# Optimization experiments

Hardware: AMD Instinct MI355X
Metric: run time of the kernel (lower is better)

The kernel has to match this reference:

```python
import jax, jax.numpy as jnp
import numpy as np

IMG_H = IMG_W = 640.0
NB, NE, NA = 120, 8, 12
L_OBJ, L_BOX, L_HEAD, L_ATTR = 1.0, 5.0, 2.0, 1.0
IGN = -100


def _smooth_l1(p, t):
    d = jnp.abs(p - t)
    return jnp.where(d < 1.0, 0.5 * d * d, d - 0.5)


def _safe_ce(logits, tgt, num_classes):
    # cross-entropy per object, zero where target == ignore_index
    logp = jax.nn.log_softmax(logits, axis=-1)
    ts = jnp.clip(tgt, 0, num_classes - 1).astype(jnp.int32)
    ce = -jnp.take_along_axis(logp, ts[..., None], axis=-1)[..., 0]
    return jnp.where(tgt == IGN, 0.0, ce)


def _scale_box(bx):
    # boxes with max coord <= 1.5 are normalized -> scale to pixels
    sc = jnp.array([IMG_W, IMG_H, IMG_W, IMG_H], dtype=bx.dtype)
    is_norm = jnp.max(bx, axis=-1, keepdims=True) <= 1.5
    return jnp.where(is_norm, bx * sc, bx)


def _per_scale(pred, body_boxes, head_boxes, labels, emotions, actions, head_valid):
    B, H, W, _ = pred.shape
    N = body_boxes.shape[1]
    sx, sy = IMG_W / W, IMG_H / H

    bb = _scale_box(body_boxes)
    x1, y1, x2, y2 = bb[..., 0], bb[..., 1], bb[..., 2], bb[..., 3]
    bw, bh = x2 - x1, y2 - y1
    cx, cy = 0.5 * (x1 + x2), 0.5 * (y1 + y2)
    gx = jnp.floor(cx / sx).astype(jnp.int32)
    gy = jnp.floor(cy / sy).astype(jnp.int32)
    valid = (bw > 0) & (bh > 0) & (gx >= 0) & (gy >= 0) & (gx < W) & (gy < H)

    # smaller-area objects claim grid cells first (argsort priority in torch loop)
    area = jnp.clip(body_boxes[..., 2] - body_boxes[..., 0], 0, None) * \
           jnp.clip(body_boxes[..., 3] - body_boxes[..., 1], 0, None)
    rank = jnp.argsort(jnp.argsort(area, axis=1), axis=1)
    rank_eff = jnp.where(valid, rank, N + 1)

    gxc, gyc = jnp.clip(gx, 0, W - 1), jnp.clip(gy, 0, H - 1)
    cell = (jnp.arange(B)[:, None] * H + gyc) * W + gxc  # [B,N] flat cell id
    min_rank = jnp.full((B * H * W,), N + 2, dtype=rank.dtype).at[cell.reshape(-1)].min(rank_eff.reshape(-1))
    winner = valid & (rank_eff == min_rank[cell])
    wf = winner.astype(pred.dtype)
    pos = winner.sum()

    bi = jnp.arange(B)[:, None]
    cp = pred[bi, gyc, gxc]  # [B,N,C] gathered cell predictions

    bw_s = jnp.where(winner, bw, sx)
    bh_s = jnp.where(winner, bh, sy)
    t_xy = jax.lax.stop_gradient(jnp.stack([cx / sx - gx, cy / sy - gy], -1))
    t_wh = jax.lax.stop_gradient(jnp.stack([jnp.log(bw_s / sx + 1e-6), jnp.log(bh_s / sy + 1e-6)], -1))
    pred_xy = jax.nn.sigmoid(cp[..., 1:3])
    pred_wh = cp[..., 3:5]
    box_l = (_smooth_l1(pred_xy, t_xy).sum(-1) + _smooth_l1(pred_wh, t_wh).sum(-1)) * wf

    hb = _scale_box(head_boxes)
    hx1, hy1, hx2, hy2 = hb[..., 0], hb[..., 1], hb[..., 2], hb[..., 3]
    hmask = winner & head_valid & (hx2 > hx1) & (hy2 > hy1)
    rel = jnp.stack([(hx1 - x1) / bw_s, (hy1 - y1) / bh_s,
                     (hx2 - x1) / bw_s, (hy2 - y1) / bh_s], -1)
    rel = jax.lax.stop_gradient(jnp.clip(rel, 0.0, 1.0))
    head_l = _smooth_l1(jax.nn.sigmoid(cp[..., 5:9]), rel).sum(-1) * hmask.astype(pred.dtype)

    # attribute cross-entropies
    off = 9
    attr_l = (_safe_ce(cp[..., off:off + NB], labels, NB)
              + _safe_ce(cp[..., off + NB:off + NB + NE], emotions, NE)
              + _safe_ce(cp[..., off + NB + NE:off + NB + NE + NA], actions, NA)) * wf

    # full-grid objectness BCE-with-logits (softplus(x) - x*t)
    obj = pred[..., 0]
    obj_target = jax.lax.stop_gradient(jnp.zeros((B, H, W), pred.dtype).at[bi, gyc, gxc].add(wf))
    bce = (jax.nn.softplus(obj) - obj * obj_target).sum()

    loss = L_BOX * box_l.sum() + L_HEAD * head_l.sum() + L_ATTR * attr_l.sum() + L_OBJ * bce
    return loss, pos


def setup_inputs() -> dict:
    key = jax.random.key(0)
    ks = jax.random.split(key, 12)
    B, N, C = 16, 24, 9 + NB + NE + NA
    pred0 = jax.random.normal(ks[0], (B, 80, 80, C), jnp.float32) * 0.5
    pred1 = jax.random.normal(ks[1], (B, 40, 40, C), jnp.float32) * 0.5
    pred2 = jax.random.normal(ks[2], (B, 20, 20, C), jnp.float32) * 0.5

    cx = jax.random.uniform(ks[3], (B, N)) * 0.8 + 0.1
    cy = jax.random.uniform(ks[4], (B, N)) * 0.8 + 0.1
    w = jax.random.uniform(ks[5], (B, N)) * 0.25 + 0.03
    h = jax.random.uniform(ks[6], (B, N)) * 0.25 + 0.03
    body = jnp.clip(jnp.stack([cx - w / 2, cy - h / 2, cx + w / 2, cy + h / 2], -1), 1e-3, 0.999)
    degen = jnp.arange(N) >= N - 4  # last 4 objects per image are padding (zero-area)
    body_boxes = jnp.where(degen[None, :, None], 0.0, body)

    # head boxes: shrunk boxes near the body top
    head = jnp.clip(jnp.stack([cx - w / 4, cy - h / 2, cx + w / 4, cy - h / 8], -1), 1e-3, 0.999)
    head_boxes = jnp.where(degen[None, :, None], 0.0, head)

    labels = jax.random.randint(ks[7], (B, N), 0, NB, jnp.int32)
    labels = jnp.where(jax.random.uniform(ks[8], (B, N)) < 0.1, IGN, labels)  # exercise ignore_index
    emotions = jax.random.randint(ks[9], (B, N), 0, NE, jnp.int32)
    actions = jax.random.randint(ks[10], (B, N), 0, NA, jnp.int32)
    head_valid = jax.random.uniform(ks[11], (B, N)) < 0.8
    return {"pred0": pred0, "pred1": pred1, "pred2": pred2,
            "body_boxes": body_boxes, "head_boxes": head_boxes,
            "labels": labels, "emotions": emotions, "actions": actions,
            "head_valid": head_valid}


def reference(pred0, pred1, pred2, body_boxes, head_boxes, labels, emotions, actions, head_valid):
    total = jnp.float32(0.0)
    pos = jnp.int32(0)
    for pred in (pred0, pred1, pred2):
        l, p = _per_scale(pred, body_boxes, head_boxes, labels, emotions, actions, head_valid)
        total = total + l
        pos = pos + p
    return total / jnp.maximum(pos, 1)
```

## Files before the change

kernel.cpp:

```cpp
#include <hip/hip_runtime.h>

#define IMG 640.0f
#define NBOX 24
#define BATCH 16
#define NB 120
#define NE 8
#define NA 12
#define C_CH 149
#define IGN_LBL (-100)

#define OBJ_TOTAL 134400
#define OBJ_BLOCKS 525
#define WIN_BLOCKS 48

__device__ __forceinline__ float softplusf_(float x) {
    return fmaxf(x, 0.0f) + log1pf(expf(-fabsf(x)));
}
__device__ __forceinline__ float sigmoidf_(float x) {
    return 1.0f / (1.0f + expf(-x));
}
__device__ __forceinline__ float smooth_l1(float p, float t) {
    float d = fabsf(p - t);
    return (d < 1.0f) ? 0.5f * d * d : d - 0.5f;
}
__device__ __forceinline__ float ce_loss(const float* __restrict__ logits, int K, int tgt) {
    if (tgt == IGN_LBL) return 0.0f;
    int ts = min(max(tgt, 0), K - 1);
    float m = -INFINITY;
    for (int i = 0; i < K; ++i) m = fmaxf(m, logits[i]);
    float s = 0.0f;
    for (int i = 0; i < K; ++i) s += expf(logits[i] - m);
    return m + logf(s) - logits[ts];
}

__global__ __launch_bounds__(256) void yolo_main(
    const float* __restrict__ p0, const float* __restrict__ p1, const float* __restrict__ p2,
    const float* __restrict__ body, const float* __restrict__ headb,
    const int* __restrict__ labels, const int* __restrict__ emotions,
    const int* __restrict__ actions, const void* __restrict__ head_valid,
    float* __restrict__ loss_acc, int* __restrict__ pos_acc)
{
    __shared__ float redf[4];
    __shared__ int   redi[4];
    __shared__ float sh_x1[NBOX], sh_y1[NBOX], sh_x2[NBOX], sh_y2[NBOX], sh_area[NBOX];
    __shared__ int   sh_cell[NBOX], sh_rank[NBOX], sh_valid[NBOX], sh_mode;

    const int blk = blockIdx.x;
    const int t = threadIdx.x;
    float v_loss = 0.0f;
    int   v_pos  = 0;

    if (blk < OBJ_BLOCKS) {
        int idx = blk * 256 + t;
        const float* p; int cell;
        if (idx < 102400)      { p = p0; cell = idx; }
        else if (idx < 128000) { p = p1; cell = idx - 102400; }
        else                   { p = p2; cell = idx - 128000; }
        v_loss = softplusf_(p[(size_t)cell * C_CH]);
    } else {
        int wb = blk - OBJ_BLOCKS;
        int s = wb >> 4, b = wb & 15;
        int W = (s == 0) ? 80 : (s == 1) ? 40 : 20;
        const float* pred = (s == 0) ? p0 : (s == 1) ? p1 : p2;
        float sc = IMG / (float)W;

        if (t == 0) {
            const unsigned* w = (const unsigned*)head_valid;
            int u8 = 0;
            for (int i = 0; i < (BATCH * NBOX) / 4; ++i)
                if (w[i] > 1u) u8 = 1;
            sh_mode = u8;
        }
        if (t < NBOX) {
            const float* bb = body + ((size_t)b * NBOX + t) * 4;
            float b0 = bb[0], b1 = bb[1], b2 = bb[2], b3 = bb[3];
            float mx = fmaxf(fmaxf(b0, b1), fmaxf(b2, b3));
            float f  = (mx <= 1.5f) ? IMG : 1.0f;
            float x1 = b0 * f, y1 = b1 * f, x2 = b2 * f, y2 = b3 * f;
            float bw = x2 - x1, bh = y2 - y1;
            float cx = 0.5f * (x1 + x2), cy = 0.5f * (y1 + y2);
            int gx = (int)floorf(cx / sc), gy = (int)floorf(cy / sc);
            int valid = (bw > 0.0f) && (bh > 0.0f) && (gx >= 0) && (gy >= 0) && (gx < W) && (gy < W);
            float area = fmaxf(b2 - b0, 0.0f) * fmaxf(b3 - b1, 0.0f);
            int gxc = min(max(gx, 0), W - 1), gyc = min(max(gy, 0), W - 1);
            sh_x1[t] = x1; sh_y1[t] = y1; sh_x2[t] = x2; sh_y2[t] = y2;
            sh_area[t] = area; sh_cell[t] = gyc * W + gxc; sh_valid[t] = valid;
        }
        __syncthreads();
        if (t < NBOX) {
            float a = sh_area[t];
            int r = 0;
            for (int j = 0; j < NBOX; ++j) {
                float aj = sh_area[j];
                if (aj < a || (aj == a && j < t)) r++;
            }
            sh_rank[t] = sh_valid[t] ? r : (NBOX + 1);
        }
        __syncthreads();
        if (t < NBOX && sh_valid[t]) {
            int r = sh_rank[t], c = sh_cell[t];
            bool win = true;
            for (int j = 0; j < NBOX; ++j)
                if (sh_cell[j] == c && sh_rank[j] < r) win = false;
            if (win) {
                v_pos = 1;
                int gy = c / W, gx = c - gy * W;
                const float* cp = pred + ((size_t)(b * W + gy) * W + gx) * C_CH;
                float x1 = sh_x1[t], y1 = sh_y1[t], x2 = sh_x2[t], y2 = sh_y2[t];
                float bw = x2 - x1, bh = y2 - y1;
                float cx = 0.5f * (x1 + x2), cy = 0.5f * (y1 + y2);
                float tx = cx / sc - (float)gx;
                float ty = cy / sc - (float)gy;
                float tw = logf(bw / sc + 1e-6f);
                float th = logf(bh / sc + 1e-6f);
                float c0 = cp[0];
                float box_l = smooth_l1(sigmoidf_(cp[1]), tx) + smooth_l1(sigmoidf_(cp[2]), ty)
                            + smooth_l1(cp[3], tw) + smooth_l1(cp[4], th);
                const float* hb = headb + ((size_t)b * NBOX + t) * 4;
                float h0 = hb[0], h1 = hb[1], h2 = hb[2], h3 = hb[3];
                float hmx = fmaxf(fmaxf(h0, h1), fmaxf(h2, h3));
                float hf  = (hmx <= 1.5f) ? IMG : 1.0f;
                float hx1 = h0 * hf, hy1 = h1 * hf, hx2 = h2 * hf, hy2 = h3 * hf;
                int li = b * NBOX + t;
                int hv = sh_mode ? (((const unsigned char*)head_valid)[li] != 0)
                                 : (((const int*)head_valid)[li] != 0);
                float head_l = 0.0f;
                if (hv && hx2 > hx1 && hy2 > hy1) {
                    float r0 = fminf(fmaxf((hx1 - x1) / bw, 0.0f), 1.0f);
                    float r1 = fminf(fmaxf((hy1 - y1) / bh, 0.0f), 1.0f);
                    float r2 = fminf(fmaxf((hx2 - x1) / bw, 0.0f), 1.0f);
                    float r3 = fminf(fmaxf((hy2 - y1) / bh, 0.0f), 1.0f);
                    head_l = smooth_l1(sigmoidf_(cp[5]), r0) + smooth_l1(sigmoidf_(cp[6]), r1)
                           + smooth_l1(sigmoidf_(cp[7]), r2) + smooth_l1(sigmoidf_(cp[8]), r3);
                }
                float attr_l = ce_loss(cp + 9, NB, labels[li])
                             + ce_loss(cp + 9 + NB, NE, emotions[li])
                             + ce_loss(cp + 9 + NB + NE, NA, actions[li]);
                v_loss = 5.0f * box_l + 2.0f * head_l + attr_l - c0;
            }
        }
    }

    for (int o = 32; o > 0; o >>= 1) {
        v_loss += __shfl_down(v_loss, o);
        v_pos  += __shfl_down(v_pos, o);
    }
    int lane = t & 63, wid = t >> 6;
    if (lane == 0) { redf[wid] = v_loss; redi[wid] = v_pos; }
    __syncthreads();
    if (t == 0) {
        float L = redf[0] + redf[1] + redf[2] + redf[3];
        int   P = redi[0] + redi[1] + redi[2] + redi[3];
        atomicAdd(loss_acc, L);
        if (P) atomicAdd(pos_acc, P);
    }
}

__global__ void yolo_finalize(const float* __restrict__ loss_acc,
                              const int* __restrict__ pos_acc,
                              float* __restrict__ out)
{
    out[0] = loss_acc[0] / (float)max(pos_acc[0], 1);
}

extern "C" void kernel_launch(void* const* d_in, const int* in_sizes, int n_in,
                              void* d_out, int out_size, void* d_ws, size_t ws_size,
                              hipStream_t stream) {
    const float* p0      = (const float*)d_in[0];
    const float* p1      = (const float*)d_in[1];
    const float* p2      = (const float*)d_in[2];
    const float* body    = (const float*)d_in[3];
    const float* headb   = (const float*)d_in[4];
    const int*   labels  = (const int*)d_in[5];
    const int*   emotions= (const int*)d_in[6];
    const int*   actions = (const int*)d_in[7];
    const void*  hvalid  = d_in[8];

    float* loss_acc = (float*)d_ws;
    int*   pos_acc  = (int*)d_ws + 1;

    hipMemsetAsync(d_ws, 0, 8, stream);
    yolo_main<<<OBJ_BLOCKS + WIN_BLOCKS, 256, 0, stream>>>(
        p0, p1, p2, body, headb, labels, emotions, actions, hvalid, loss_acc, pos_acc);
    yolo_finalize<<<1, 1, 0, stream>>>(loss_acc, pos_acc, (float*)d_out);
}
```

Baseline: 143.7 us.

## Spread per-object loss across wavefront lanes with shuffle reductions for softmax

Winner-object loss evaluation moves from a single thread per object, which looped serially over 149 channels for three cross-entropies, to a whole 64-lane wavefront per object. Each wavefront handles 6 objects, loads the channels coalesced and computes the max/sum for the three softmaxes with xor-shuffle reductions. Per-object targets (box offsets, head ratios, labels) are precomputed into shared memory, which adds a sync and more shared state. The goal is to shorten the serial tail in the 48 winner blocks, which otherwise delay kernel completion.

```diff
diff --git a/kernel.cpp b/kernel.cpp
--- a/kernel.cpp
+++ b/kernel.cpp
@@ -9,7 +9,6 @@
 #define C_CH 149
 #define IGN_LBL (-100)
 
-#define OBJ_TOTAL 134400
 #define OBJ_BLOCKS 525
 #define WIN_BLOCKS 48
 
@@ -22,15 +21,6 @@
 __device__ __forceinline__ float smooth_l1(float p, float t) {
     float d = fabsf(p - t);
     return (d < 1.0f) ? 0.5f * d * d : d - 0.5f;
-}
-__device__ __forceinline__ float ce_loss(const float* __restrict__ logits, int K, int tgt) {
-    if (tgt == IGN_LBL) return 0.0f;
-    int ts = min(max(tgt, 0), K - 1);
-    float m = -INFINITY;
-    for (int i = 0; i < K; ++i) m = fmaxf(m, logits[i]);
-    float s = 0.0f;
-    for (int i = 0; i < K; ++i) s += expf(logits[i] - m);
-    return m + logf(s) - logits[ts];
 }
 
 __global__ __launch_bounds__(256) void yolo_main(
@@ -42,8 +32,12 @@
 {
     __shared__ float redf[4];
     __shared__ int   redi[4];
-    __shared__ float sh_x1[NBOX], sh_y1[NBOX], sh_x2[NBOX], sh_y2[NBOX], sh_area[NBOX];
-    __shared__ int   sh_cell[NBOX], sh_rank[NBOX], sh_valid[NBOX], sh_mode;
+    __shared__ float s_tx[NBOX], s_ty[NBOX], s_tw[NBOX], s_th[NBOX];
+    __shared__ float s_r0[NBOX], s_r1[NBOX], s_r2[NBOX], s_r3[NBOX];
+    __shared__ float s_area[NBOX];
+    __shared__ int   s_cell[NBOX], s_rank[NBOX], s_valid[NBOX], s_win[NBOX], s_hm[NBOX];
+    __shared__ int   s_lab[NBOX], s_emo[NBOX], s_act[NBOX], s_off[NBOX];
+    __shared__ int   sh_mode;
 
     const int blk = blockIdx.x;
     const int t = threadIdx.x;
@@ -71,8 +65,10 @@
                 if (w[i] > 1u) u8 = 1;
             sh_mode = u8;
         }
+        __syncthreads();
         if (t < NBOX) {
-            const float* bb = body + ((size_t)b * NBOX + t) * 4;
+            int li = b * NBOX + t;
+            const float* bb = body + (size_t)li * 4;
             float b0 = bb[0], b1 = bb[1], b2 = bb[2], b3 = bb[3];
             float mx = fmaxf(fmaxf(b0, b1), fmaxf(b2, b3));
             float f  = (mx <= 1.5f) ? IMG : 1.0f;
@@ -83,62 +79,123 @@
             int valid = (bw > 0.0f) && (bh > 0.0f) && (gx >= 0) && (gy >= 0) && (gx < W) && (gy < W);
             float area = fmaxf(b2 - b0, 0.0f) * fmaxf(b3 - b1, 0.0f);
             int gxc = min(max(gx, 0), W - 1), gyc = min(max(gy, 0), W - 1);
-            sh_x1[t] = x1; sh_y1[t] = y1; sh_x2[t] = x2; sh_y2[t] = y2;
-            sh_area[t] = area; sh_cell[t] = gyc * W + gxc; sh_valid[t] = valid;
+            s_area[t] = area; s_cell[t] = gyc * W + gxc; s_valid[t] = valid;
+            s_off[t]  = ((b * W + gyc) * W + gxc) * C_CH;
+            s_tx[t] = cx / sc - (float)gx;
+            s_ty[t] = cy / sc - (float)gy;
+            s_tw[t] = logf(fmaxf(bw / sc, 0.0f) + 1e-6f);
+            s_th[t] = logf(fmaxf(bh / sc, 0.0f) + 1e-6f);
+            const float* hb = headb + (size_t)li * 4;
+            float h0 = hb[0], h1 = hb[1], h2 = hb[2], h3 = hb[3];
+            float hmx = fmaxf(fmaxf(h0, h1), fmaxf(h2, h3));
+            float hf  = (hmx <= 1.5f) ? IMG : 1.0f;
+            float hx1 = h0 * hf, hy1 = h1 * hf, hx2 = h2 * hf, hy2 = h3 * hf;
+            int hv = sh_mode ? (((const unsigned char*)head_valid)[li] != 0)
+                             : (((const int*)head_valid)[li] != 0);
+            s_hm[t] = hv && (hx2 > hx1) && (hy2 > hy1);
+            float rb = (bw > 0.0f) ? bw : 1.0f;
+            float rh = (bh > 0.0f) ? bh : 1.0f;
+            s_r0[t] = fminf(fmaxf((hx1 - x1) / rb, 0.0f), 1.0f);
+            s_r1[t] = fminf(fmaxf((hy1 - y1) / rh, 0.0f), 1.0f);
+            s_r2[t] = fminf(fmaxf((hx2 - x1) / rb, 0.0f), 1.0f);
+            s_r3[t] = fminf(fmaxf((hy2 - y1) / rh, 0.0f), 1.0f);
+            s_lab[t] = labels[li]; s_emo[t] = emotions[li]; s_act[t] = actions[li];
         }
         __syncthreads();
         if (t < NBOX) {
-            float a = sh_area[t];
+            float a = s_area[t];
             int r = 0;
             for (int j = 0; j < NBOX; ++j) {
-                float aj = sh_area[j];
+                float aj = s_area[j];
                 if (aj < a || (aj == a && j < t)) r++;
             }
-            sh_rank[t] = sh_valid[t] ? r : (NBOX + 1);
-        }
-        __syncthreads();
-        if (t < NBOX && sh_valid[t]) {
-            int r = sh_rank[t], c = sh_cell[t];
-            bool win = true;
-            for (int j = 0; j < NBOX; ++j)
-                if (sh_cell[j] == c && sh_rank[j] < r) win = false;
-            if (win) {
-                v_pos = 1;
-                int gy = c / W, gx = c - gy * W;
-                const float* cp = pred + ((size_t)(b * W + gy) * W + gx) * C_CH;
-                float x1 = sh_x1[t], y1 = sh_y1[t], x2 = sh_x2[t], y2 = sh_y2[t];
-                float bw = x2 - x1, bh = y2 - y1;
-                float cx = 0.5f * (x1 + x2), cy = 0.5f * (y1 + y2);
-                float tx = cx / sc - (float)gx;
-                float ty = cy / sc - (float)gy;
-                float tw = logf(bw / sc + 1e-6f);
-                float th = logf(bh / sc + 1e-6f);
-                float c0 = cp[0];
-                float box_l = smooth_l1(sigmoidf_(cp[1]), tx) + smooth_l1(sigmoidf_(cp[2]), ty)
-                            + smooth_l1(cp[3], tw) + smooth_l1(cp[4], th);
-                const float* hb = headb + ((size_t)b * NBOX + t) * 4;
-                float h0 = hb[0], h1 = hb[1], h2 = hb[2], h3 = hb[3];
-                float hmx = fmaxf(fmaxf(h0, h1), fmaxf(h2, h3));
-                float hf  = (hmx <= 1.5f) ? IMG : 1.0f;
-                float hx1 = h0 * hf, hy1 = h1 * hf, hx2 = h2 * hf, hy2 = h3 * hf;
-                int li = b * NBOX + t;
-                int hv = sh_mode ? (((const unsigned char*)head_valid)[li] != 0)
-                                 : (((const int*)head_valid)[li] != 0);
-                float head_l = 0.0f;
-                if (hv && hx2 > hx1 && hy2 > hy1) {
-                    float r0 = fminf(fmaxf((hx1 - x1) / bw, 0.0f), 1.0f);
-                    float r1 = fminf(fmaxf((hy1 - y1) / bh, 0.0f), 1.0f);
-                    float r2 = fminf(fmaxf((hx2 - x1) / bw, 0.0f), 1.0f);
-                    float r3 = fminf(fmaxf((hy2 - y1) / bh, 0.0f), 1.0f);
-                    head_l = smooth_l1(sigmoidf_(cp[5]), r0) + smooth_l1(sigmoidf_(cp[6]), r1)
-                           + smooth_l1(sigmoidf_(cp[7]), r2) + smooth_l1(sigmoidf_(cp[8]), r3);
+            s_rank[t] = s_valid[t] ? r : (NBOX + 1);
+        }
+        __syncthreads();
+        if (t < NBOX) {
+            int win = 0;
+            if (s_valid[t]) {
+                int r = s_rank[t], c = s_cell[t];
+                win = 1;
+                for (int j = 0; j < NBOX; ++j)
+                    if (s_cell[j] == c && s_rank[j] < r) win = 0;
+            }
+            s_win[t] = win;
+            v_pos = win;
+        }
+        __syncthreads();
+        int w = t >> 6, lane = t & 63;
+        float wacc = 0.0f;
+        for (int k = 0; k < 6; ++k) {
+            int i = w * 6 + k;
+            if (!s_win[i]) continue;
+            const float* cp = pred + s_off[i];
+            float q0 = cp[lane];
+            float q1 = cp[64 + lane];
+            float q2 = (lane < 21) ? cp[128 + lane] : -1e30f;
+            float mNB = (lane >= 9) ? q0 : -1e30f;
+            mNB = fmaxf(mNB, q1);
+            if (lane == 0) mNB = fmaxf(mNB, q2);
+            float mNE = (lane >= 1 && lane <= 8)  ? q2 : -1e30f;
+            float mNA = (lane >= 9 && lane <= 20) ? q2 : -1e30f;
+            #pragma unroll
+            for (int m = 1; m < 64; m <<= 1) {
+                mNB = fmaxf(mNB, __shfl_xor(mNB, m));
+                mNE = fmaxf(mNE, __shfl_xor(mNE, m));
+                mNA = fmaxf(mNA, __shfl_xor(mNA, m));
+            }
+            float sNB = (lane >= 9) ? expf(q0 - mNB) : 0.0f;
+            sNB += expf(q1 - mNB);
+            if (lane == 0) sNB += expf(q2 - mNB);
+            float sNE = (lane >= 1 && lane <= 8)  ? expf(q2 - mNE) : 0.0f;
+            float sNA = (lane >= 9 && lane <= 20) ? expf(q2 - mNA) : 0.0f;
+
+            float ctr = 0.0f;
+            if (lane == 0)      ctr -= q0;
+            else if (lane == 1) ctr += 5.0f * smooth_l1(sigmoidf_(q0), s_tx[i]);
+            else if (lane == 2) ctr += 5.0f * smooth_l1(sigmoidf_(q0), s_ty[i]);
+            else if (lane == 3) ctr += 5.0f * smooth_l1(q0, s_tw[i]);
+            else if (lane == 4) ctr += 5.0f * smooth_l1(q0, s_th[i]);
+            else if (lane >= 5 && lane <= 8) {
+                if (s_hm[i]) {
+                    float tg = (lane == 5) ? s_r0[i] : (lane == 6) ? s_r1[i]
+                             : (lane == 7) ? s_r2[i] : s_r3[i];
+                    ctr += 2.0f * smooth_l1(sigmoidf_(q0), tg);
                 }
-                float attr_l = ce_loss(cp + 9, NB, labels[li])
-                             + ce_loss(cp + 9 + NB, NE, emotions[li])
-                             + ce_loss(cp + 9 + NB + NE, NA, actions[li]);
-                v_loss = 5.0f * box_l + 2.0f * head_l + attr_l - c0;
-            }
-        }
+            }
+            int lab = s_lab[i];
+            if (lab != IGN_LBL) {
+                int ix = 9 + min(max(lab, 0), NB - 1);
+                if (ix < 64)       { if (lane == ix)       ctr -= q0; }
+                else if (ix < 128) { if (lane == ix - 64)  ctr -= q1; }
+                else               { if (lane == 0)        ctr -= q2; }
+            }
+            int emo = s_emo[i];
+            if (emo != IGN_LBL) {
+                int ix = 129 + min(max(emo, 0), NE - 1);
+                if (lane == ix - 128) ctr -= q2;
+            }
+            int act = s_act[i];
+            if (act != IGN_LBL) {
+                int ix = 137 + min(max(act, 0), NA - 1);
+                if (lane == ix - 128) ctr -= q2;
+            }
+            #pragma unroll
+            for (int m = 1; m < 64; m <<= 1) {
+                sNB += __shfl_xor(sNB, m);
+                sNE += __shfl_xor(sNE, m);
+                sNA += __shfl_xor(sNA, m);
+                ctr += __shfl_xor(ctr, m);
+            }
+            if (lane == 0) {
+                float add = ctr;
+                if (lab != IGN_LBL) add += mNB + logf(sNB);
+                if (emo != IGN_LBL) add += mNE + logf(sNE);
+                if (act != IGN_LBL) add += mNA + logf(sNA);
+                wacc += add;
+            }
+        }
+        if (lane == 0) v_loss = wacc;
     }
 
     for (int o = 32; o > 0; o >>= 1) {
```

Result: faster. 133.0 us (-7.5%).
